# Performance work log

Hardware: AMD Instinct MI355X
Metric: run time of the kernel (lower is better)

Reference implementation:

```python
import jax, jax.numpy as jnp
import numpy as np

B, T, D = 32, 512, 64
P = 16          # token_t_size
OV = 8          # token_t_overlap
DM = 512        # d_model
STRIDE = P - OV
NW = (T - P) // STRIDE + 1  # 63 windows per channel


def setup_inputs() -> dict:
    key = jax.random.key(0)
    k0, k1, k2, k3, k4 = jax.random.split(key, 5)
    x = jax.random.normal(k0, (B, T, D), jnp.float32)
    Wt = jax.random.normal(k1, (DM, P), jnp.float32) / np.sqrt(P).astype(np.float32)
    bt = jax.random.normal(k2, (DM,), jnp.float32) * 0.01
    Wd = jax.random.normal(k3, (DM, D), jnp.float32) / np.sqrt(D).astype(np.float32)
    bd = jax.random.normal(k4, (DM,), jnp.float32) * 0.01
    return {"x": x, "Wt": Wt, "bt": bt, "Wd": Wd, "bd": bd}


def reference(x, Wt, bt, Wd, bd):
    # Sliding windows: starts = 0, stride, 2*stride, ...
    starts = jnp.arange(NW) * STRIDE                    # [NW]
    idx = starts[:, None] + jnp.arange(P)               # [NW, P]
    patches = x[:, idx, :]                              # [B, NW, P, D]
    # Original loop order: d outer, window inner -> token = d*NW + w
    temporal = jnp.einsum('bwpd,mp->bdwm', patches, Wt) + bt  # [B, D, NW, DM]
    temporal = temporal.reshape(B, D * NW, DM)
    # Feature tokens: per-timestep Linear(D -> DM) == one batched matmul
    feature = jnp.einsum('btd,md->btm', x, Wd) + bd     # [B, T, DM]
    return jnp.concatenate([temporal, feature], axis=1)  # [B, D*NW + T, DM]
```

## Files before the change

### kernel.cpp

```cpp
#include <hip/hip_runtime.h>
#include <cstddef>
#include <cstdint>

namespace {

constexpr int kB = 32, kT = 512, kD = 64, kP = 16, kNW = 63, kDM = 512;
constexpr int kRows = kD * kNW + kT;
constexpr int kSS = 516;

typedef float f32x4  __attribute__((ext_vector_type(4)));
typedef short bf16x8 __attribute__((ext_vector_type(8)));

constexpr int kWdOff = 32768;

__device__ __forceinline__ unsigned short bf16_rne(float f) {
    unsigned int u = __float_as_uint(f);
    u += 0x7fffu + ((u >> 16) & 1u);
    return (unsigned short)(u >> 16);
}
__device__ __forceinline__ float bf16_f(unsigned short h) {
    return __uint_as_float(((unsigned int)h) << 16);
}

__global__ __launch_bounds__(256)
void prep_k(const float* __restrict__ Wt, const float* __restrict__ Wd,
            unsigned short* __restrict__ ws)
{
    const int gid = blockIdx.x * 256 + threadIdx.x;
    for (int e = gid; e < 32 * 64; e += gridDim.x * 256) {
        const int n = e >> 6, l = e & 63;
        unsigned short* dh = ws + ((size_t)(n * 2 + 0) * 64 + l) * 8;
        unsigned short* dl = ws + ((size_t)(n * 2 + 1) * 64 + l) * 8;
        if (l < 32) {
            const int row = 16 * n + (l & 15);
            const int p0  = 8 * (l >> 4);
            #pragma unroll
            for (int j = 0; j < 8; ++j) {
                float f = Wt[row * kP + p0 + j];
                unsigned short h = bf16_rne(f);
                dh[j] = h;
                dl[j] = bf16_rne(f - bf16_f(h));
            }
        } else {
            #pragma unroll
            for (int j = 0; j < 8; ++j) { dh[j] = 0; dl[j] = 0; }
        }
    }
    for (int e = gid; e < 32 * 2 * 64; e += gridDim.x * 256) {
        const int n = e >> 7, kc = (e >> 6) & 1, l = e & 63;
        const int row = 16 * n + (l & 15);
        const int d0  = 32 * kc + 8 * (l >> 4);
        unsigned short* dh = ws + kWdOff + ((size_t)((n * 2 + kc) * 2 + 0) * 64 + l) * 8;
        unsigned short* dl = ws + kWdOff + ((size_t)((n * 2 + kc) * 2 + 1) * 64 + l) * 8;
        #pragma unroll
        for (int j = 0; j < 8; ++j) {
            float f = Wd[row * kD + d0 + j];
            unsigned short h = bf16_rne(f);
            dh[j] = h;
            dl[j] = bf16_rne(f - bf16_f(h));
        }
    }
}

__global__ __launch_bounds__(256)
void temporal_k(const float* __restrict__ x, const unsigned short* __restrict__ ws,
                const float* __restrict__ bt, float* __restrict__ out)
{
    __shared__ __align__(16) unsigned short hi_s[640];
    __shared__ __align__(16) unsigned short lo_s[640];
    __shared__ __align__(16) float slab[16 * kSS];
    const int tid = threadIdx.x, lane = tid & 63, wave = tid >> 6;
    const int b = blockIdx.x >> 6, d = blockIdx.x & (kD - 1);

    #pragma unroll
    for (int i = 0; i < 2; ++i) {
        const int t = tid + 256 * i;
        const float f = x[(b * kT + t) * kD + d];
        const unsigned short h = bf16_rne(f);
        hi_s[t] = h;
        lo_s[t] = bf16_rne(f - bf16_f(h));
    }
    if (tid < 128) { hi_s[512 + tid] = 0; lo_s[512 + tid] = 0; }
    __syncthreads();

    bf16x8 Ah[8], Al[8];
    #pragma unroll
    for (int i = 0; i < 8; ++i) {
        const int n = 8 * wave + i;
        Ah[i] = *(const bf16x8*)(ws + ((n * 2 + 0) * 64 + lane) * 8);
        Al[i] = *(const bf16x8*)(ws + ((n * 2 + 1) * 64 + lane) * 8);
    }

    const int chsub  = 4 * (lane >> 4);
    const int wrbase = (lane & 15) * kSS + chsub;
    float* orow = out + (size_t)b * kRows * kDM + (size_t)(d * kNW) * kDM;

    for (int g = 0; g < 4; ++g) {
        const int toff = 128 * g + 8 * (lane & 15) + 8 * (lane >> 4);
        const bf16x8 Bh = *(const bf16x8*)(hi_s + toff);
        const bf16x8 Bl = *(const bf16x8*)(lo_s + toff);

        #pragma unroll
        for (int i = 0; i < 8; ++i) {
            const int n = 8 * wave + i;
            f32x4 acc = {0.f, 0.f, 0.f, 0.f};
            acc = __builtin_amdgcn_mfma_f32_16x16x32_bf16(Ah[i], Bh, acc, 0, 0, 0);
            acc = __builtin_amdgcn_mfma_f32_16x16x32_bf16(Al[i], Bh, acc, 0, 0, 0);
            acc = __builtin_amdgcn_mfma_f32_16x16x32_bf16(Ah[i], Bl, acc, 0, 0, 0);
            const f32x4 bias = *(const f32x4*)(bt + 16 * n + chsub);
            *(f32x4*)(slab + wrbase + 16 * n) = acc + bias;
        }
        __syncthreads();

        #pragma unroll
        for (int r = 0; r < 4; ++r) {
            const int srow = 4 * wave + r;
            const int wrow = 16 * g + srow;
            if (wrow < kNW) {
                #pragma unroll
                for (int h = 0; h < 2; ++h) {
                    const f32x4 v = *(const f32x4*)(slab + srow * kSS + h * 256 + lane * 4);
                    *(f32x4*)(orow + (size_t)wrow * kDM + h * 256 + lane * 4) = v;
                }
            }
        }
        __syncthreads();
    }
}

__global__ __launch_bounds__(256)
void feature_k(const float* __restrict__ x, const unsigned short* __restrict__ ws,
               const float* __restrict__ bd, float* __restrict__ out)
{
    __shared__ __align__(16) float slab[16 * kSS];
    const int tid = threadIdx.x, lane = tid & 63, wave = tid >> 6;
    const int b = blockIdx.x >> 5, tc = blockIdx.x & 31;
    const int t  = tc * 16 + (lane & 15);
    const int d0 = 8 * (lane >> 4);

    const float* xrow = x + ((size_t)b * kT + t) * kD;
    bf16x8 Bh[2], Bl[2];
    #pragma unroll
    for (int kc = 0; kc < 2; ++kc) {
        #pragma unroll
        for (int j = 0; j < 8; ++j) {
            const float f = xrow[32 * kc + d0 + j];
            const unsigned short h = bf16_rne(f);
            Bh[kc][j] = (short)h;
            Bl[kc][j] = (short)bf16_rne(f - bf16_f(h));
        }
    }

    const int chsub  = 4 * (lane >> 4);
    const int wrbase = (lane & 15) * kSS + chsub;
    const unsigned short* wsd = ws + kWdOff;

    #pragma unroll
    for (int i = 0; i < 8; ++i) {
        const int n = 8 * wave + i;
        const bf16x8 Ah0 = *(const bf16x8*)(wsd + (((n * 2 + 0) * 2 + 0) * 64 + lane) * 8);
        const bf16x8 Al0 = *(const bf16x8*)(wsd + (((n * 2 + 0) * 2 + 1) * 64 + lane) * 8);
        const bf16x8 Ah1 = *(const bf16x8*)(wsd + (((n * 2 + 1) * 2 + 0) * 64 + lane) * 8);
        const bf16x8 Al1 = *(const bf16x8*)(wsd + (((n * 2 + 1) * 2 + 1) * 64 + lane) * 8);
        f32x4 acc = {0.f, 0.f, 0.f, 0.f};
        acc = __builtin_amdgcn_mfma_f32_16x16x32_bf16(Ah0, Bh[0], acc, 0, 0, 0);
        acc = __builtin_amdgcn_mfma_f32_16x16x32_bf16(Al0, Bh[0], acc, 0, 0, 0);
        acc = __builtin_amdgcn_mfma_f32_16x16x32_bf16(Ah0, Bl[0], acc, 0, 0, 0);
        acc = __builtin_amdgcn_mfma_f32_16x16x32_bf16(Ah1, Bh[1], acc, 0, 0, 0);
        acc = __builtin_amdgcn_mfma_f32_16x16x32_bf16(Al1, Bh[1], acc, 0, 0, 0);
        acc = __builtin_amdgcn_mfma_f32_16x16x32_bf16(Ah1, Bl[1], acc, 0, 0, 0);
        const f32x4 bias = *(const f32x4*)(bd + 16 * n + chsub);
        *(f32x4*)(slab + wrbase + 16 * n) = acc + bias;
    }
    __syncthreads();

    float* orows = out + (size_t)b * kRows * kDM + (size_t)(kD * kNW + tc * 16) * kDM;
    #pragma unroll
    for (int r = 0; r < 4; ++r) {
        const int srow = 4 * wave + r;
        #pragma unroll
        for (int h = 0; h < 2; ++h) {
            const f32x4 v = *(const f32x4*)(slab + srow * kSS + h * 256 + lane * 4);
            *(f32x4*)(orows + (size_t)srow * kDM + h * 256 + lane * 4) = v;
        }
    }
}

}

extern "C" void kernel_launch(void* const* d_in, const int* in_sizes, int n_in,
                              void* d_out, int out_size, void* d_ws, size_t ws_size,
                              hipStream_t stream) {
    const float* x  = (const float*)d_in[0];
    const float* Wt = (const float*)d_in[1];
    const float* bt = (const float*)d_in[2];
    const float* Wd = (const float*)d_in[3];
    const float* bd = (const float*)d_in[4];
    float* out = (float*)d_out;
    unsigned short* ws = (unsigned short*)d_ws;

    hipLaunchKernelGGL(prep_k,     dim3(8),            dim3(256), 0, stream, Wt, Wd, ws);
    hipLaunchKernelGGL(temporal_k, dim3(kB * kD),      dim3(256), 0, stream, x, ws, bt, out);
    hipLaunchKernelGGL(feature_k,  dim3(kB * (kT/16)), dim3(256), 0, stream, x, ws, bd, out);
}
```

Before: 68.98 us.

## Merge temporal and feature kernels into one launch, add bias at store

```diff
diff --git a/kernel.cpp b/kernel.cpp
--- a/kernel.cpp
+++ b/kernel.cpp
@@ -7,6 +7,8 @@
 constexpr int kB = 32, kT = 512, kD = 64, kP = 16, kNW = 63, kDM = 512;
 constexpr int kRows = kD * kNW + kT;
 constexpr int kSS = 516;
+constexpr int kNBF = kB * (kT / 16);
+constexpr int kNBT = kB * kD;
 
 typedef float f32x4  __attribute__((ext_vector_type(4)));
 typedef short bf16x8 __attribute__((ext_vector_type(8)));
@@ -63,125 +65,130 @@
 }
 
 __global__ __launch_bounds__(256)
-void temporal_k(const float* __restrict__ x, const unsigned short* __restrict__ ws,
-                const float* __restrict__ bt, float* __restrict__ out)
+void main_k(const float* __restrict__ x, const unsigned short* __restrict__ ws,
+            const float* __restrict__ bt, const float* __restrict__ bd,
+            float* __restrict__ out)
 {
+    __shared__ __align__(16) float slab[16 * kSS];
     __shared__ __align__(16) unsigned short hi_s[640];
     __shared__ __align__(16) unsigned short lo_s[640];
-    __shared__ __align__(16) float slab[16 * kSS];
     const int tid = threadIdx.x, lane = tid & 63, wave = tid >> 6;
-    const int b = blockIdx.x >> 6, d = blockIdx.x & (kD - 1);
-
-    #pragma unroll
-    for (int i = 0; i < 2; ++i) {
-        const int t = tid + 256 * i;
-        const float f = x[(b * kT + t) * kD + d];
-        const unsigned short h = bf16_rne(f);
-        hi_s[t] = h;
-        lo_s[t] = bf16_rne(f - bf16_f(h));
-    }
-    if (tid < 128) { hi_s[512 + tid] = 0; lo_s[512 + tid] = 0; }
-    __syncthreads();
-
-    bf16x8 Ah[8], Al[8];
-    #pragma unroll
-    for (int i = 0; i < 8; ++i) {
-        const int n = 8 * wave + i;
-        Ah[i] = *(const bf16x8*)(ws + ((n * 2 + 0) * 64 + lane) * 8);
-        Al[i] = *(const bf16x8*)(ws + ((n * 2 + 1) * 64 + lane) * 8);
-    }
-
-    const int chsub  = 4 * (lane >> 4);
-    const int wrbase = (lane & 15) * kSS + chsub;
-    float* orow = out + (size_t)b * kRows * kDM + (size_t)(d * kNW) * kDM;
-
-    for (int g = 0; g < 4; ++g) {
-        const int toff = 128 * g + 8 * (lane & 15) + 8 * (lane >> 4);
-        const bf16x8 Bh = *(const bf16x8*)(hi_s + toff);
-        const bf16x8 Bl = *(const bf16x8*)(lo_s + toff);
-
+
+    if ((int)blockIdx.x >= kNBF) {
+        const int blk = blockIdx.x - kNBF;
+        const int b = blk >> 6, d = blk & (kD - 1);
+
+        #pragma unroll
+        for (int i = 0; i < 2; ++i) {
+            const int t = tid + 256 * i;
+            const float f = x[(b * kT + t) * kD + d];
+            const unsigned short h = bf16_rne(f);
+            hi_s[t] = h;
+            lo_s[t] = bf16_rne(f - bf16_f(h));
+        }
+        if (tid < 128) { hi_s[512 + tid] = 0; lo_s[512 + tid] = 0; }
+        __syncthreads();
+
+        bf16x8 Ah[8], Al[8];
         #pragma unroll
         for (int i = 0; i < 8; ++i) {
             const int n = 8 * wave + i;
+            Ah[i] = *(const bf16x8*)(ws + ((n * 2 + 0) * 64 + lane) * 8);
+            Al[i] = *(const bf16x8*)(ws + ((n * 2 + 1) * 64 + lane) * 8);
+        }
+
+        f32x4 biasw[2];
+        biasw[0] = *(const f32x4*)(bt + lane * 4);
+        biasw[1] = *(const f32x4*)(bt + 256 + lane * 4);
+
+        const int chsub  = 4 * (lane >> 4);
+        const int wrbase = (lane & 15) * kSS + chsub;
+        float* orow = out + (size_t)b * kRows * kDM + (size_t)(d * kNW) * kDM;
+
+        for (int g = 0; g < 4; ++g) {
+            const int toff = 128 * g + 8 * (lane & 15) + 8 * (lane >> 4);
+            const bf16x8 Bh = *(const bf16x8*)(hi_s + toff);
+            const bf16x8 Bl = *(const bf16x8*)(lo_s + toff);
+
+            #pragma unroll
+            for (int i = 0; i < 8; ++i) {
+                const int n = 8 * wave + i;
+                f32x4 acc = {0.f, 0.f, 0.f, 0.f};
+                acc = __builtin_amdgcn_mfma_f32_16x16x32_bf16(Ah[i], Bh, acc, 0, 0, 0);
+                acc = __builtin_amdgcn_mfma_f32_16x16x32_bf16(Al[i], Bh, acc, 0, 0, 0);
+                acc = __builtin_amdgcn_mfma_f32_16x16x32_bf16(Ah[i], Bl, acc, 0, 0, 0);
+                *(f32x4*)(slab + wrbase + 16 * n) = acc;
+            }
+            __syncthreads();
+
+            #pragma unroll
+            for (int r = 0; r < 4; ++r) {
+                const int srow = 4 * wave + r;
+                const int wrow = 16 * g + srow;
+                if (wrow < kNW) {
+                    #pragma unroll
+                    for (int h = 0; h < 2; ++h) {
+                        const f32x4 v = *(const f32x4*)(slab + srow * kSS + h * 256 + lane * 4);
+                        *(f32x4*)(orow + (size_t)wrow * kDM + h * 256 + lane * 4) = v + biasw[h];
+                    }
+                }
+            }
+            __syncthreads();
+        }
+    } else {
+        const int blk = blockIdx.x;
+        const int b = blk >> 5, tc = blk & 31;
+        const int t  = tc * 16 + (lane & 15);
+        const int d0 = 8 * (lane >> 4);
+
+        const float* xrow = x + ((size_t)b * kT + t) * kD;
+        bf16x8 Bh[2], Bl[2];
+        #pragma unroll
+        for (int kc = 0; kc < 2; ++kc) {
+            #pragma unroll
+            for (int j = 0; j < 8; ++j) {
+                const float f = xrow[32 * kc + d0 + j];
+                const unsigned short h = bf16_rne(f);
+                Bh[kc][j] = (short)h;
+                Bl[kc][j] = (short)bf16_rne(f - bf16_f(h));
+            }
+        }
+
+        f32x4 biasw[2];
+        biasw[0] = *(const f32x4*)(bd + lane * 4);
+        biasw[1] = *(const f32x4*)(bd + 256 + lane * 4);
+
+        const int chsub  = 4 * (lane >> 4);
+        const int wrbase = (lane & 15) * kSS + chsub;
+        const unsigned short* wsd = ws + kWdOff;
+
+        #pragma unroll
+        for (int i = 0; i < 8; ++i) {
+            const int n = 8 * wave + i;
+            const bf16x8 Ah0 = *(const bf16x8*)(wsd + (((n * 2 + 0) * 2 + 0) * 64 + lane) * 8);
+            const bf16x8 Al0 = *(const bf16x8*)(wsd + (((n * 2 + 0) * 2 + 1) * 64 + lane) * 8);
+            const bf16x8 Ah1 = *(const bf16x8*)(wsd + (((n * 2 + 1) * 2 + 0) * 64 + lane) * 8);
+            const bf16x8 Al1 = *(const bf16x8*)(wsd + (((n * 2 + 1) * 2 + 1) * 64 + lane) * 8);
             f32x4 acc = {0.f, 0.f, 0.f, 0.f};
-            acc = __builtin_amdgcn_mfma_f32_16x16x32_bf16(Ah[i], Bh, acc, 0, 0, 0);
-            acc = __builtin_amdgcn_mfma_f32_16x16x32_bf16(Al[i], Bh, acc, 0, 0, 0);
-            acc = __builtin_amdgcn_mfma_f32_16x16x32_bf16(Ah[i], Bl, acc, 0, 0, 0);
-            const f32x4 bias = *(const f32x4*)(bt + 16 * n + chsub);
-            *(f32x4*)(slab + wrbase + 16 * n) = acc + bias;
+            acc = __builtin_amdgcn_mfma_f32_16x16x32_bf16(Ah0, Bh[0], acc, 0, 0, 0);
+            acc = __builtin_amdgcn_mfma_f32_16x16x32_bf16(Al0, Bh[0], acc, 0, 0, 0);
+            acc = __builtin_amdgcn_mfma_f32_16x16x32_bf16(Ah0, Bl[0], acc, 0, 0, 0);
+            acc = __builtin_amdgcn_mfma_f32_16x16x32_bf16(Ah1, Bh[1], acc, 0, 0, 0);
+            acc = __builtin_amdgcn_mfma_f32_16x16x32_bf16(Al1, Bh[1], acc, 0, 0, 0);
+            acc = __builtin_amdgcn_mfma_f32_16x16x32_bf16(Ah1, Bl[1], acc, 0, 0, 0);
+            *(f32x4*)(slab + wrbase + 16 * n) = acc;
         }
         __syncthreads();
 
+        float* orows = out + (size_t)b * kRows * kDM + (size_t)(kD * kNW + tc * 16) * kDM;
         #pragma unroll
         for (int r = 0; r < 4; ++r) {
             const int srow = 4 * wave + r;
-            const int wrow = 16 * g + srow;
-            if (wrow < kNW) {
-                #pragma unroll
-                for (int h = 0; h < 2; ++h) {
-                    const f32x4 v = *(const f32x4*)(slab + srow * kSS + h * 256 + lane * 4);
-                    *(f32x4*)(orow + (size_t)wrow * kDM + h * 256 + lane * 4) = v;
-                }
-            }
-        }
-        __syncthreads();
-    }
-}
-
-__global__ __launch_bounds__(256)
-void feature_k(const float* __restrict__ x, const unsigned short* __restrict__ ws,
-               const float* __restrict__ bd, float* __restrict__ out)
-{
-    __shared__ __align__(16) float slab[16 * kSS];
-    const int tid = threadIdx.x, lane = tid & 63, wave = tid >> 6;
-    const int b = blockIdx.x >> 5, tc = blockIdx.x & 31;
-    const int t  = tc * 16 + (lane & 15);
-    const int d0 = 8 * (lane >> 4);
-
-    const float* xrow = x + ((size_t)b * kT + t) * kD;
-    bf16x8 Bh[2], Bl[2];
-    #pragma unroll
-    for (int kc = 0; kc < 2; ++kc) {
-        #pragma unroll
-        for (int j = 0; j < 8; ++j) {
-            const float f = xrow[32 * kc + d0 + j];
-            const unsigned short h = bf16_rne(f);
-            Bh[kc][j] = (short)h;
-            Bl[kc][j] = (short)bf16_rne(f - bf16_f(h));
-        }
-    }
-
-    const int chsub  = 4 * (lane >> 4);
-    const int wrbase = (lane & 15) * kSS + chsub;
-    const unsigned short* wsd = ws + kWdOff;
-
-    #pragma unroll
-    for (int i = 0; i < 8; ++i) {
-        const int n = 8 * wave + i;
-        const bf16x8 Ah0 = *(const bf16x8*)(wsd + (((n * 2 + 0) * 2 + 0) * 64 + lane) * 8);
-        const bf16x8 Al0 = *(const bf16x8*)(wsd + (((n * 2 + 0) * 2 + 1) * 64 + lane) * 8);
-        const bf16x8 Ah1 = *(const bf16x8*)(wsd + (((n * 2 + 1) * 2 + 0) * 64 + lane) * 8);
-        const bf16x8 Al1 = *(const bf16x8*)(wsd + (((n * 2 + 1) * 2 + 1) * 64 + lane) * 8);
-        f32x4 acc = {0.f, 0.f, 0.f, 0.f};
-        acc = __builtin_amdgcn_mfma_f32_16x16x32_bf16(Ah0, Bh[0], acc, 0, 0, 0);
-        acc = __builtin_amdgcn_mfma_f32_16x16x32_bf16(Al0, Bh[0], acc, 0, 0, 0);
-        acc = __builtin_amdgcn_mfma_f32_16x16x32_bf16(Ah0, Bl[0], acc, 0, 0, 0);
-        acc = __builtin_amdgcn_mfma_f32_16x16x32_bf16(Ah1, Bh[1], acc, 0, 0, 0);
-        acc = __builtin_amdgcn_mfma_f32_16x16x32_bf16(Al1, Bh[1], acc, 0, 0, 0);
-        acc = __builtin_amdgcn_mfma_f32_16x16x32_bf16(Ah1, Bl[1], acc, 0, 0, 0);
-        const f32x4 bias = *(const f32x4*)(bd + 16 * n + chsub);
-        *(f32x4*)(slab + wrbase + 16 * n) = acc + bias;
-    }
-    __syncthreads();
-
-    float* orows = out + (size_t)b * kRows * kDM + (size_t)(kD * kNW + tc * 16) * kDM;
-    #pragma unroll
-    for (int r = 0; r < 4; ++r) {
-        const int srow = 4 * wave + r;
-        #pragma unroll
-        for (int h = 0; h < 2; ++h) {
-            const f32x4 v = *(const f32x4*)(slab + srow * kSS + h * 256 + lane * 4);
-            *(f32x4*)(orows + (size_t)srow * kDM + h * 256 + lane * 4) = v;
+            #pragma unroll
+            for (int h = 0; h < 2; ++h) {
+                const f32x4 v = *(const f32x4*)(slab + srow * kSS + h * 256 + lane * 4);
+                *(f32x4*)(orows + (size_t)srow * kDM + h * 256 + lane * 4) = v + biasw[h];
+            }
         }
     }
 }
@@ -199,7 +206,6 @@
     float* out = (float*)d_out;
     unsigned short* ws = (unsigned short*)d_ws;
 
-    hipLaunchKernelGGL(prep_k,     dim3(8),            dim3(256), 0, stream, Wt, Wd, ws);
-    hipLaunchKernelGGL(temporal_k, dim3(kB * kD),      dim3(256), 0, stream, x, ws, bt, out);
-    hipLaunchKernelGGL(feature_k,  dim3(kB * (kT/16)), dim3(256), 0, stream, x, ws, bd, out);
-}
+    hipLaunchKernelGGL(prep_k, dim3(16),           dim3(256), 0, stream, Wt, Wd, ws);
+    hipLaunchKernelGGL(main_k, dim3(kNBF + kNBT),  dim3(256), 0, stream, x, ws, bt, bd, out);
+}
```

Result: faster. 64.52 us (-6.5%).
